# Kernel optimization log

Hardware: AMD Instinct MI355X
Metric: run time of the kernel (lower is better)

Reference implementation:

```python
import jax, jax.numpy as jnp
import numpy as np

B, N, L, M, F = 32, 32, 512, 64, 64
EPS = 1e-8

def setup_inputs() -> dict:
    key = jax.random.key(0)
    k1, k2, k3, k4, k5 = jax.random.split(key, 5)
    x_aug = jax.random.normal(k1, (B, N, L, F), dtype=jnp.float32)
    # monotone time grid in [0,1], shape (L,1) so it broadcasts against (1,N,1,M)
    t = jnp.linspace(0.0, 1.0, L, dtype=jnp.float32)[:, None]
    t_left = jax.random.uniform(k2, (N, M), dtype=jnp.float32) * 0.8
    t_right = t_left + 0.05 + 0.15 * jax.random.uniform(k3, (N, M), dtype=jnp.float32)
    kappa = jax.random.normal(k4, (N, 1), dtype=jnp.float32)
    return {"x_aug": x_aug, "t": t, "t_left": t_left, "t_right": t_right, "kappa": kappa}

def reference(x_aug, t, t_left, t_right, kappa):
    # kappa: (N,1) -> softplus -> (1,N,1,1)
    k = jax.nn.softplus(kappa)[None, :, None]          # (1,N,1,1)
    tl = t_left[None, :, None, :]                       # (1,N,1,M)
    tr = t_right[None, :, None, :]                      # (1,N,1,M)
    # soft box kernel over time: alpha (1,N,L,M)
    alpha = jax.nn.sigmoid((tr - t) / k) * jax.nn.sigmoid((t - tl) / k)
    # weighted pool over L without materializing (B,N,L,M,F)
    numerator = jnp.einsum('bnlf,nlm->bnmf', x_aug, alpha[0])  # (B,N,M,F)
    denominator = alpha.sum(axis=2)[..., None]                 # (1,N,M,1)
    return numerator / (denominator + EPS)
```

## Files before the change

### kernel.cpp

```cpp
#include <hip/hip_runtime.h>
#include <math.h>

typedef unsigned short u16;
typedef unsigned int   u32;
typedef __attribute__((ext_vector_type(8))) short short8;
typedef __attribute__((ext_vector_type(4))) float f32x4;

namespace {
constexpr int Bb = 32, Nn = 32, Ll = 512, Mm = 64, Ff = 64;
constexpr int TL  = 32;
constexpr int NT  = Ll / TL;
constexpr int TLP = 40;
constexpr float EPSV = 1e-8f;
}

__device__ __forceinline__ u16 bf16rne(float x) {
    u32 u = __float_as_uint(x);
    return (u16)((u + 0x7fffu + ((u >> 16) & 1u)) >> 16);
}
__device__ __forceinline__ float bf16tof(u16 h) {
    return __uint_as_float(((u32)h) << 16);
}

__global__ __launch_bounds__(256, 4)
void wagg_fused(const float* __restrict__ x_aug,
                const float* __restrict__ t_in,
                const float* __restrict__ t_left,
                const float* __restrict__ t_right,
                const float* __restrict__ kappa,
                float* __restrict__ out)
{
    const int n   = blockIdx.x & 31;
    const int b   = blockIdx.x >> 5;
    const int tid = threadIdx.x;

    __shared__ u16 ah_s[2][Mm * TLP];
    __shared__ u16 al_s[2][Mm * TLP];
    __shared__ u16 xh_s[2][Ff * TLP];
    __shared__ u16 xl_s[2][Ff * TLP];

    const int fq  = tid & 15;
    const int lp2 = tid >> 4;

    const int wv   = tid >> 6;
    const int lane = tid & 63;
    const int ma   = wv * 16 + (lane >> 2);
    const int lqa  = lane & 3;

    const int mh = wv & 1;
    const int fh = wv >> 1;
    const int q  = lane >> 4;
    const int c  = lane & 15;

    const float* xb = x_aug + (size_t)(b * Nn + n) * (Ll * Ff);

    const float kap = kappa[n];
    const float kk  = fmaxf(kap, 0.0f) + log1pf(expf(-fabsf(kap)));
    const float ik  = 1.0f / kk;
    const float tlv = t_left [n * Mm + ma];
    const float trv = t_right[n * Mm + ma];
    const float Ac  = __expf(-trv * ik);
    const float Bc  = __expf( tlv * ik);

    f32x4 acc[2][2];
    #pragma unroll
    for (int mi = 0; mi < 2; ++mi)
        #pragma unroll
        for (int fi = 0; fi < 2; ++fi)
            acc[mi][fi] = (f32x4){0.f, 0.f, 0.f, 0.f};

    float X0[4], X1[4];
    float T[8];
    float dsum = 0.0f;

    auto stage = [&](int buf) {
        #pragma unroll
        for (int j = 0; j < 4; ++j) {
            const float v0 = X0[j], v1 = X1[j];
            const u16 h0 = bf16rne(v0), h1 = bf16rne(v1);
            const u16 s0 = bf16rne(v0 - bf16tof(h0)), s1 = bf16rne(v1 - bf16tof(h1));
            const u32 off = (u32)(fq * 4 + j) * TLP + 2 * lp2;
            *(u32*)&xh_s[buf][off] = (u32)h0 | ((u32)h1 << 16);
            *(u32*)&xl_s[buf][off] = (u32)s0 | ((u32)s1 << 16);
        }
        u32 hi[4], lo[4];
        #pragma unroll
        for (int jj = 0; jj < 8; jj += 2) {
            const float u0 = __expf(T[jj]     * ik);
            const float u1 = __expf(T[jj + 1] * ik);
            const float d0 = fmaf(Ac, u0, 1.0f) * (u0 + Bc);
            const float d1 = fmaf(Ac, u1, 1.0f) * (u1 + Bc);
            const float a0 = u0 * __builtin_amdgcn_rcpf(d0);
            const float a1 = u1 * __builtin_amdgcn_rcpf(d1);
            dsum += a0 + a1;
            const u16 h0 = bf16rne(a0), h1 = bf16rne(a1);
            const u16 s0 = bf16rne(a0 - bf16tof(h0)), s1 = bf16rne(a1 - bf16tof(h1));
            hi[jj >> 1] = (u32)h0 | ((u32)h1 << 16);
            lo[jj >> 1] = (u32)s0 | ((u32)s1 << 16);
        }
        const u32 aoff = (u32)ma * TLP + lqa * 8;
        *(uint4*)&ah_s[buf][aoff] = make_uint4(hi[0], hi[1], hi[2], hi[3]);
        *(uint4*)&al_s[buf][aoff] = make_uint4(lo[0], lo[1], lo[2], lo[3]);
    };

    {
        const float* p = xb + (size_t)(2 * lp2) * Ff + fq * 4;
        *(float4*)X0 = *(const float4*)p;
        *(float4*)X1 = *(const float4*)(p + Ff);
        *(float4*)&T[0] = *(const float4*)&t_in[lqa * 8];
        *(float4*)&T[4] = *(const float4*)&t_in[lqa * 8 + 4];
        stage(0);
    }
    __syncthreads();

    for (int tile = 0; tile < NT; ++tile) {
        const int cur = tile & 1, nxt = cur ^ 1;

        if (tile + 1 < NT) {
            const int l0 = (tile + 1) * TL;
            const float* p = xb + (size_t)(l0 + 2 * lp2) * Ff + fq * 4;
            *(float4*)X0 = *(const float4*)p;
            *(float4*)X1 = *(const float4*)(p + Ff);
            *(float4*)&T[0] = *(const float4*)&t_in[l0 + lqa * 8];
            *(float4*)&T[4] = *(const float4*)&t_in[l0 + lqa * 8 + 4];
        }

        short8 ahf[2], alf[2], xhf[2], xlf[2];
        #pragma unroll
        for (int mi = 0; mi < 2; ++mi) {
            const u32 off = (u32)(mh * 32 + mi * 16 + c) * TLP + q * 8;
            ahf[mi] = *(const short8*)&ah_s[cur][off];
            alf[mi] = *(const short8*)&al_s[cur][off];
        }
        #pragma unroll
        for (int fi = 0; fi < 2; ++fi) {
            const u32 off = (u32)(fh * 32 + fi * 16 + c) * TLP + q * 8;
            xhf[fi] = *(const short8*)&xh_s[cur][off];
            xlf[fi] = *(const short8*)&xl_s[cur][off];
        }
        #pragma unroll
        for (int mi = 0; mi < 2; ++mi)
            #pragma unroll
            for (int fi = 0; fi < 2; ++fi) {
                acc[mi][fi] = __builtin_amdgcn_mfma_f32_16x16x32_bf16(
                    ahf[mi], xhf[fi], acc[mi][fi], 0, 0, 0);
                acc[mi][fi] = __builtin_amdgcn_mfma_f32_16x16x32_bf16(
                    ahf[mi], xlf[fi], acc[mi][fi], 0, 0, 0);
                acc[mi][fi] = __builtin_amdgcn_mfma_f32_16x16x32_bf16(
                    alf[mi], xhf[fi], acc[mi][fi], 0, 0, 0);
            }

        if (tile + 1 < NT) stage(nxt);
        __syncthreads();
    }

    float* dred = (float*)&xh_s[0][0];
    float* invp = dred + 256;
    dred[lqa * 64 + ma] = dsum;
    __syncthreads();
    if (tid < Mm) {
        const float d = dred[tid] + dred[64 + tid] + dred[128 + tid] + dred[192 + tid];
        invp[tid] = __builtin_amdgcn_rcpf(d + EPSV);
    }
    __syncthreads();

    float* ob = out + (size_t)(b * Nn + n) * (Mm * Ff);
    #pragma unroll
    for (int mi = 0; mi < 2; ++mi) {
        const int mbase = mh * 32 + mi * 16 + q * 4;
        float iv[4];
        #pragma unroll
        for (int r = 0; r < 4; ++r) iv[r] = invp[mbase + r];
        #pragma unroll
        for (int fi = 0; fi < 2; ++fi) {
            const int f = fh * 32 + fi * 16 + c;
            #pragma unroll
            for (int r = 0; r < 4; ++r)
                ob[(size_t)(mbase + r) * Ff + f] = acc[mi][fi][r] * iv[r];
        }
    }
}

extern "C" void kernel_launch(void* const* d_in, const int* in_sizes, int n_in,
                              void* d_out, int out_size, void* d_ws, size_t ws_size,
                              hipStream_t stream)
{
    const float* x_aug   = (const float*)d_in[0];
    const float* t_in    = (const float*)d_in[1];
    const float* t_left  = (const float*)d_in[2];
    const float* t_right = (const float*)d_in[3];
    const float* kappa   = (const float*)d_in[4];
    float* out = (float*)d_out;

    hipLaunchKernelGGL(wagg_fused, dim3(Bb * Nn), dim3(256), 0, stream,
                       x_aug, t_in, t_left, t_right, kappa, out);
}
```

Measured before the change: 205.9 us.

## Precompute alpha split-bf16 tiles in separate kernel and stream them from global memory

Splits the fused kernel in two. A small per-n kernel computes the sigmoid-product weights once, stores them as hi/lo bf16 in an MFMA-fragment-friendly global layout, and stores the reciprocal denominators. The main kernel then loads those fragments directly from global (L2-resident) instead of recomputing alpha in every batch block. It also adds an XOR swizzle on the x LDS tiles, a two-deep register prefetch of x, and a lighter lgkm-only barrier. The cost is an extra launch and a small global workspace round trip, with the fused kernel kept as a fallback when no workspace is provided.

```diff
diff --git a/kernel.cpp b/kernel.cpp
--- a/kernel.cpp
+++ b/kernel.cpp
@@ -12,6 +12,7 @@
 constexpr int NT  = Ll / TL;
 constexpr int TLP = 40;
 constexpr float EPSV = 1e-8f;
+constexpr size_t A_ELEMS = (size_t)Nn * Ll * Mm;
 }
 
 __device__ __forceinline__ u16 bf16rne(float x) {
@@ -22,37 +23,26 @@
     return __uint_as_float(((u32)h) << 16);
 }
 
+__device__ __forceinline__ void lgkm_barrier() {
+    asm volatile("s_waitcnt lgkmcnt(0)" ::: "memory");
+    __builtin_amdgcn_s_barrier();
+    asm volatile("" ::: "memory");
+}
+
 __global__ __launch_bounds__(256, 4)
-void wagg_fused(const float* __restrict__ x_aug,
-                const float* __restrict__ t_in,
+void wagg_alpha(const float* __restrict__ t_in,
                 const float* __restrict__ t_left,
                 const float* __restrict__ t_right,
                 const float* __restrict__ kappa,
-                float* __restrict__ out)
+                u16* __restrict__ Ahi, u16* __restrict__ Alo,
+                float* __restrict__ inv_g)
 {
-    const int n   = blockIdx.x & 31;
-    const int b   = blockIdx.x >> 5;
+    const int n   = blockIdx.x;
     const int tid = threadIdx.x;
-
-    __shared__ u16 ah_s[2][Mm * TLP];
-    __shared__ u16 al_s[2][Mm * TLP];
-    __shared__ u16 xh_s[2][Ff * TLP];
-    __shared__ u16 xl_s[2][Ff * TLP];
-
-    const int fq  = tid & 15;
-    const int lp2 = tid >> 4;
-
-    const int wv   = tid >> 6;
-    const int lane = tid & 63;
-    const int ma   = wv * 16 + (lane >> 2);
-    const int lqa  = lane & 3;
-
-    const int mh = wv & 1;
-    const int fh = wv >> 1;
-    const int q  = lane >> 4;
-    const int c  = lane & 15;
-
-    const float* xb = x_aug + (size_t)(b * Nn + n) * (Ll * Ff);
+    const int ma  = tid >> 2;
+    const int lqa = tid & 3;
+
+    __shared__ float dred[256];
 
     const float kap = kappa[n];
     const float kk  = fmaxf(kap, 0.0f) + log1pf(expf(-fabsf(kap)));
@@ -62,27 +52,11 @@
     const float Ac  = __expf(-trv * ik);
     const float Bc  = __expf( tlv * ik);
 
-    f32x4 acc[2][2];
-    #pragma unroll
-    for (int mi = 0; mi < 2; ++mi)
-        #pragma unroll
-        for (int fi = 0; fi < 2; ++fi)
-            acc[mi][fi] = (f32x4){0.f, 0.f, 0.f, 0.f};
-
-    float X0[4], X1[4];
-    float T[8];
     float dsum = 0.0f;
-
-    auto stage = [&](int buf) {
-        #pragma unroll
-        for (int j = 0; j < 4; ++j) {
-            const float v0 = X0[j], v1 = X1[j];
-            const u16 h0 = bf16rne(v0), h1 = bf16rne(v1);
-            const u16 s0 = bf16rne(v0 - bf16tof(h0)), s1 = bf16rne(v1 - bf16tof(h1));
-            const u32 off = (u32)(fq * 4 + j) * TLP + 2 * lp2;
-            *(u32*)&xh_s[buf][off] = (u32)h0 | ((u32)h1 << 16);
-            *(u32*)&xl_s[buf][off] = (u32)s0 | ((u32)s1 << 16);
-        }
+    for (int t = 0; t < NT; ++t) {
+        float T[8];
+        *(float4*)&T[0] = *(const float4*)&t_in[t * TL + lqa * 8];
+        *(float4*)&T[4] = *(const float4*)&t_in[t * TL + lqa * 8 + 4];
         u32 hi[4], lo[4];
         #pragma unroll
         for (int jj = 0; jj < 8; jj += 2) {
@@ -98,6 +72,201 @@
             hi[jj >> 1] = (u32)h0 | ((u32)h1 << 16);
             lo[jj >> 1] = (u32)s0 | ((u32)s1 << 16);
         }
+        const size_t off = ((((size_t)n * NT + t) * 4 + lqa) * Mm + ma) * 8;
+        *(uint4*)&Ahi[off] = make_uint4(hi[0], hi[1], hi[2], hi[3]);
+        *(uint4*)&Alo[off] = make_uint4(lo[0], lo[1], lo[2], lo[3]);
+    }
+
+    dred[lqa * 64 + ma] = dsum;
+    __syncthreads();
+    if (tid < Mm) {
+        const float d = dred[tid] + dred[64 + tid] + dred[128 + tid] + dred[192 + tid];
+        inv_g[n * Mm + tid] = __builtin_amdgcn_rcpf(d + EPSV);
+    }
+}
+
+__global__ __launch_bounds__(256, 4)
+void wagg_main(const float* __restrict__ x_aug,
+               const u16* __restrict__ Ahi, const u16* __restrict__ Alo,
+               const float* __restrict__ inv_g,
+               float* __restrict__ out)
+{
+    const int n   = blockIdx.x & 31;
+    const int b   = blockIdx.x >> 5;
+    const int tid = threadIdx.x;
+
+    __shared__ u16 xh_s[2][Ff * TLP];
+    __shared__ u16 xl_s[2][Ff * TLP];
+
+    const int fq  = tid & 15;
+    const int lp2 = tid >> 4;
+    const int sw   = (fq >> 1) & 3;
+    const u32 wbase = (u32)(((lp2 >> 2) ^ sw) * 8 + (lp2 & 3) * 2);
+
+    const int wv = tid >> 6, lane = tid & 63;
+    const int mh = wv & 1;
+    const int fh = wv >> 1;
+    const int q  = lane >> 4;
+    const int c  = lane & 15;
+
+    const float* xb = x_aug + (size_t)(b * Nn + n) * (Ll * Ff);
+
+    f32x4 acc[2][2];
+    #pragma unroll
+    for (int mi = 0; mi < 2; ++mi)
+        #pragma unroll
+        for (int fi = 0; fi < 2; ++fi)
+            acc[mi][fi] = (f32x4){0.f, 0.f, 0.f, 0.f};
+
+    float XA0[4], XA1[4], XB0[4], XB1[4];
+
+#define LOADX(X0_, X1_, T_) { \
+    const float* p_ = xb + (size_t)((T_) * TL + 2 * lp2) * Ff + fq * 4; \
+    *(float4*)(X0_) = *(const float4*)p_; \
+    *(float4*)(X1_) = *(const float4*)(p_ + Ff); }
+
+#define STAGEX(BUF_, X0_, X1_) { \
+    _Pragma("unroll") \
+    for (int j = 0; j < 4; ++j) { \
+        const float v0 = (X0_)[j], v1 = (X1_)[j]; \
+        const u16 h0 = bf16rne(v0), h1 = bf16rne(v1); \
+        const u16 s0 = bf16rne(v0 - bf16tof(h0)), s1 = bf16rne(v1 - bf16tof(h1)); \
+        const u32 off_ = (u32)(fq * 4 + j) * TLP + wbase; \
+        *(u32*)&xh_s[BUF_][off_] = (u32)h0 | ((u32)h1 << 16); \
+        *(u32*)&xl_s[BUF_][off_] = (u32)s0 | ((u32)s1 << 16); } }
+
+#define TILE(T_, CUR_, XS0_, XS1_, XL0_, XL1_) { \
+    short8 ahf[2], alf[2], xhf[2], xlf[2]; \
+    const u16* ab_ = Ahi + ((((size_t)n * NT + (T_)) * 4 + q) * Mm) * 8; \
+    const u16* lb_ = Alo + ((((size_t)n * NT + (T_)) * 4 + q) * Mm) * 8; \
+    _Pragma("unroll") \
+    for (int mi = 0; mi < 2; ++mi) { \
+        const int row_ = mh * 32 + mi * 16 + c; \
+        ahf[mi] = *(const short8*)(ab_ + row_ * 8); \
+        alf[mi] = *(const short8*)(lb_ + row_ * 8); } \
+    if ((T_) + 2 < NT) LOADX(XL0_, XL1_, (T_) + 2); \
+    _Pragma("unroll") \
+    for (int fi = 0; fi < 2; ++fi) { \
+        const int row_ = fh * 32 + fi * 16 + c; \
+        const u32 off_ = (u32)row_ * TLP + (u32)((q ^ ((row_ >> 3) & 3)) * 8); \
+        xhf[fi] = *(const short8*)&xh_s[CUR_][off_]; \
+        xlf[fi] = *(const short8*)&xl_s[CUR_][off_]; } \
+    _Pragma("unroll") \
+    for (int mi = 0; mi < 2; ++mi) \
+        _Pragma("unroll") \
+        for (int fi = 0; fi < 2; ++fi) { \
+            acc[mi][fi] = __builtin_amdgcn_mfma_f32_16x16x32_bf16(ahf[mi], xhf[fi], acc[mi][fi], 0, 0, 0); \
+            acc[mi][fi] = __builtin_amdgcn_mfma_f32_16x16x32_bf16(ahf[mi], xlf[fi], acc[mi][fi], 0, 0, 0); \
+            acc[mi][fi] = __builtin_amdgcn_mfma_f32_16x16x32_bf16(alf[mi], xhf[fi], acc[mi][fi], 0, 0, 0); } \
+    if ((T_) + 1 < NT) STAGEX((CUR_) ^ 1, XS0_, XS1_); \
+    lgkm_barrier(); }
+
+    LOADX(XA0, XA1, 0);
+    STAGEX(0, XA0, XA1);
+    LOADX(XB0, XB1, 1);
+    lgkm_barrier();
+
+    for (int tt = 0; tt < NT / 2; ++tt) {
+        const int t0 = 2 * tt;
+        TILE(t0,     0, XB0, XB1, XA0, XA1);
+        TILE(t0 + 1, 1, XA0, XA1, XB0, XB1);
+    }
+
+#undef TILE
+#undef STAGEX
+#undef LOADX
+
+    const float* ivp = inv_g + n * Mm;
+    float* ob = out + (size_t)(b * Nn + n) * (Mm * Ff);
+    #pragma unroll
+    for (int mi = 0; mi < 2; ++mi) {
+        const int mbase = mh * 32 + mi * 16 + q * 4;
+        float iv[4];
+        *(float4*)iv = *(const float4*)&ivp[mbase];
+        #pragma unroll
+        for (int fi = 0; fi < 2; ++fi) {
+            const int f = fh * 32 + fi * 16 + c;
+            #pragma unroll
+            for (int r = 0; r < 4; ++r)
+                ob[(size_t)(mbase + r) * Ff + f] = acc[mi][fi][r] * iv[r];
+        }
+    }
+}
+
+__global__ __launch_bounds__(256, 4)
+void wagg_fused(const float* __restrict__ x_aug,
+                const float* __restrict__ t_in,
+                const float* __restrict__ t_left,
+                const float* __restrict__ t_right,
+                const float* __restrict__ kappa,
+                float* __restrict__ out)
+{
+    const int n   = blockIdx.x & 31;
+    const int b   = blockIdx.x >> 5;
+    const int tid = threadIdx.x;
+
+    __shared__ u16 ah_s[2][Mm * TLP];
+    __shared__ u16 al_s[2][Mm * TLP];
+    __shared__ u16 xh_s[2][Ff * TLP];
+    __shared__ u16 xl_s[2][Ff * TLP];
+
+    const int fq  = tid & 15;
+    const int lp2 = tid >> 4;
+    const int wv   = tid >> 6;
+    const int lane = tid & 63;
+    const int ma   = wv * 16 + (lane >> 2);
+    const int lqa  = lane & 3;
+    const int mh = wv & 1;
+    const int fh = wv >> 1;
+    const int q  = lane >> 4;
+    const int c  = lane & 15;
+
+    const float* xb = x_aug + (size_t)(b * Nn + n) * (Ll * Ff);
+
+    const float kap = kappa[n];
+    const float kk  = fmaxf(kap, 0.0f) + log1pf(expf(-fabsf(kap)));
+    const float ik  = 1.0f / kk;
+    const float tlv = t_left [n * Mm + ma];
+    const float trv = t_right[n * Mm + ma];
+    const float Ac  = __expf(-trv * ik);
+    const float Bc  = __expf( tlv * ik);
+
+    f32x4 acc[2][2];
+    #pragma unroll
+    for (int mi = 0; mi < 2; ++mi)
+        #pragma unroll
+        for (int fi = 0; fi < 2; ++fi)
+            acc[mi][fi] = (f32x4){0.f, 0.f, 0.f, 0.f};
+
+    float X0[4], X1[4];
+    float T[8];
+    float dsum = 0.0f;
+
+    auto stage = [&](int buf) {
+        #pragma unroll
+        for (int j = 0; j < 4; ++j) {
+            const float v0 = X0[j], v1 = X1[j];
+            const u16 h0 = bf16rne(v0), h1 = bf16rne(v1);
+            const u16 s0 = bf16rne(v0 - bf16tof(h0)), s1 = bf16rne(v1 - bf16tof(h1));
+            const u32 off = (u32)(fq * 4 + j) * TLP + 2 * lp2;
+            *(u32*)&xh_s[buf][off] = (u32)h0 | ((u32)h1 << 16);
+            *(u32*)&xl_s[buf][off] = (u32)s0 | ((u32)s1 << 16);
+        }
+        u32 hi[4], lo[4];
+        #pragma unroll
+        for (int jj = 0; jj < 8; jj += 2) {
+            const float u0 = __expf(T[jj]     * ik);
+            const float u1 = __expf(T[jj + 1] * ik);
+            const float d0 = fmaf(Ac, u0, 1.0f) * (u0 + Bc);
+            const float d1 = fmaf(Ac, u1, 1.0f) * (u1 + Bc);
+            const float a0 = u0 * __builtin_amdgcn_rcpf(d0);
+            const float a1 = u1 * __builtin_amdgcn_rcpf(d1);
+            dsum += a0 + a1;
+            const u16 h0 = bf16rne(a0), h1 = bf16rne(a1);
+            const u16 s0 = bf16rne(a0 - bf16tof(h0)), s1 = bf16rne(a1 - bf16tof(h1));
+            hi[jj >> 1] = (u32)h0 | ((u32)h1 << 16);
+            lo[jj >> 1] = (u32)s0 | ((u32)s1 << 16);
+        }
         const u32 aoff = (u32)ma * TLP + lqa * 8;
         *(uint4*)&ah_s[buf][aoff] = make_uint4(hi[0], hi[1], hi[2], hi[3]);
         *(uint4*)&al_s[buf][aoff] = make_uint4(lo[0], lo[1], lo[2], lo[3]);
@@ -192,6 +361,17 @@
     const float* kappa   = (const float*)d_in[4];
     float* out = (float*)d_out;
 
-    hipLaunchKernelGGL(wagg_fused, dim3(Bb * Nn), dim3(256), 0, stream,
-                       x_aug, t_in, t_left, t_right, kappa, out);
-}
+    const size_t need = 2 * A_ELEMS * sizeof(u16) + (size_t)Nn * Mm * sizeof(float);
+    if (d_ws != nullptr && ws_size >= need) {
+        u16*   Ahi   = (u16*)d_ws;
+        u16*   Alo   = Ahi + A_ELEMS;
+        float* inv_g = (float*)(Alo + A_ELEMS);
+        hipLaunchKernelGGL(wagg_alpha, dim3(Nn), dim3(256), 0, stream,
+                           t_in, t_left, t_right, kappa, Ahi, Alo, inv_g);
+        hipLaunchKernelGGL(wagg_main, dim3(Bb * Nn), dim3(256), 0, stream,
+                           x_aug, Ahi, Alo, inv_g, out);
+    } else {
+        hipLaunchKernelGGL(wagg_fused, dim3(Bb * Nn), dim3(256), 0, stream,
+                           x_aug, t_in, t_left, t_right, kappa, out);
+    }
+}
```

Result: slower. 216.7 us (+5.3%).

## Prefetch x two tiles ahead, swizzle x LDS layout, use lighter LDS-only barriers

Applied to the files above, without the earlier changes.

The kernel now issues global loads of x two tiles ahead using two alternating register sets, with the tile loop manually unrolled by two. This gives memory latency more time to hide behind the MFMA work. The LDS layout for the x hi/lo split gets an XOR swizzle on the column chunk to reduce bank conflicts on the transposed writes and fragment reads. __syncthreads is replaced with an lgkmcnt-only wait plus s_barrier, so outstanding global loads no longer drain at every barrier. The cost is higher register pressure from the extra prefetch buffers.

```diff
diff --git a/kernel.cpp b/kernel.cpp
--- a/kernel.cpp
+++ b/kernel.cpp
@@ -22,13 +22,19 @@
     return __uint_as_float(((u32)h) << 16);
 }
 
+__device__ __forceinline__ void lgkm_barrier() {
+    asm volatile("s_waitcnt lgkmcnt(0)" ::: "memory");
+    __builtin_amdgcn_s_barrier();
+    asm volatile("" ::: "memory");
+}
+
 __global__ __launch_bounds__(256, 4)
-void wagg_fused(const float* __restrict__ x_aug,
-                const float* __restrict__ t_in,
-                const float* __restrict__ t_left,
-                const float* __restrict__ t_right,
-                const float* __restrict__ kappa,
-                float* __restrict__ out)
+void wagg_fused2(const float* __restrict__ x_aug,
+                 const float* __restrict__ t_in,
+                 const float* __restrict__ t_left,
+                 const float* __restrict__ t_right,
+                 const float* __restrict__ kappa,
+                 float* __restrict__ out)
 {
     const int n   = blockIdx.x & 31;
     const int b   = blockIdx.x >> 5;
@@ -41,6 +47,8 @@
 
     const int fq  = tid & 15;
     const int lp2 = tid >> 4;
+    const int sw    = (fq >> 1) & 3;
+    const u32 wbase = (u32)(((lp2 >> 2) ^ sw) * 8 + (lp2 & 3) * 2);
 
     const int wv   = tid >> 6;
     const int lane = tid & 63;
@@ -69,100 +77,97 @@
         for (int fi = 0; fi < 2; ++fi)
             acc[mi][fi] = (f32x4){0.f, 0.f, 0.f, 0.f};
 
-    float X0[4], X1[4];
+    float XA0[4], XA1[4], XB0[4], XB1[4];
     float T[8];
     float dsum = 0.0f;
 
-    auto stage = [&](int buf) {
-        #pragma unroll
-        for (int j = 0; j < 4; ++j) {
-            const float v0 = X0[j], v1 = X1[j];
-            const u16 h0 = bf16rne(v0), h1 = bf16rne(v1);
-            const u16 s0 = bf16rne(v0 - bf16tof(h0)), s1 = bf16rne(v1 - bf16tof(h1));
-            const u32 off = (u32)(fq * 4 + j) * TLP + 2 * lp2;
-            *(u32*)&xh_s[buf][off] = (u32)h0 | ((u32)h1 << 16);
-            *(u32*)&xl_s[buf][off] = (u32)s0 | ((u32)s1 << 16);
-        }
-        u32 hi[4], lo[4];
-        #pragma unroll
-        for (int jj = 0; jj < 8; jj += 2) {
-            const float u0 = __expf(T[jj]     * ik);
-            const float u1 = __expf(T[jj + 1] * ik);
-            const float d0 = fmaf(Ac, u0, 1.0f) * (u0 + Bc);
-            const float d1 = fmaf(Ac, u1, 1.0f) * (u1 + Bc);
-            const float a0 = u0 * __builtin_amdgcn_rcpf(d0);
-            const float a1 = u1 * __builtin_amdgcn_rcpf(d1);
-            dsum += a0 + a1;
-            const u16 h0 = bf16rne(a0), h1 = bf16rne(a1);
-            const u16 s0 = bf16rne(a0 - bf16tof(h0)), s1 = bf16rne(a1 - bf16tof(h1));
-            hi[jj >> 1] = (u32)h0 | ((u32)h1 << 16);
-            lo[jj >> 1] = (u32)s0 | ((u32)s1 << 16);
-        }
-        const u32 aoff = (u32)ma * TLP + lqa * 8;
-        *(uint4*)&ah_s[buf][aoff] = make_uint4(hi[0], hi[1], hi[2], hi[3]);
-        *(uint4*)&al_s[buf][aoff] = make_uint4(lo[0], lo[1], lo[2], lo[3]);
-    };
-
-    {
-        const float* p = xb + (size_t)(2 * lp2) * Ff + fq * 4;
-        *(float4*)X0 = *(const float4*)p;
-        *(float4*)X1 = *(const float4*)(p + Ff);
-        *(float4*)&T[0] = *(const float4*)&t_in[lqa * 8];
-        *(float4*)&T[4] = *(const float4*)&t_in[lqa * 8 + 4];
-        stage(0);
+#define LOADX(X0_, X1_, T_) { \
+    const float* p_ = xb + (size_t)((T_) * TL + 2 * lp2) * Ff + fq * 4; \
+    *(float4*)(X0_) = *(const float4*)p_; \
+    *(float4*)(X1_) = *(const float4*)(p_ + Ff); }
+
+#define LOADT(T_) { \
+    *(float4*)&T[0] = *(const float4*)&t_in[(T_) * TL + lqa * 8]; \
+    *(float4*)&T[4] = *(const float4*)&t_in[(T_) * TL + lqa * 8 + 4]; }
+
+#define STAGEX(BUF_, X0_, X1_) { \
+    _Pragma("unroll") \
+    for (int j = 0; j < 4; ++j) { \
+        const float v0 = (X0_)[j], v1 = (X1_)[j]; \
+        const u16 h0 = bf16rne(v0), h1 = bf16rne(v1); \
+        const u16 s0 = bf16rne(v0 - bf16tof(h0)), s1 = bf16rne(v1 - bf16tof(h1)); \
+        const u32 off_ = (u32)(fq * 4 + j) * TLP + wbase; \
+        *(u32*)&xh_s[BUF_][off_] = (u32)h0 | ((u32)h1 << 16); \
+        *(u32*)&xl_s[BUF_][off_] = (u32)s0 | ((u32)s1 << 16); } \
+    u32 hi_[4], lo_[4]; \
+    _Pragma("unroll") \
+    for (int jj = 0; jj < 8; jj += 2) { \
+        const float u0 = __expf(T[jj]     * ik); \
+        const float u1 = __expf(T[jj + 1] * ik); \
+        const float d0 = fmaf(Ac, u0, 1.0f) * (u0 + Bc); \
+        const float d1 = fmaf(Ac, u1, 1.0f) * (u1 + Bc); \
+        const float a0 = u0 * __builtin_amdgcn_rcpf(d0); \
+        const float a1 = u1 * __builtin_amdgcn_rcpf(d1); \
+        dsum += a0 + a1; \
+        const u16 h0 = bf16rne(a0), h1 = bf16rne(a1); \
+        const u16 s0 = bf16rne(a0 - bf16tof(h0)), s1 = bf16rne(a1 - bf16tof(h1)); \
+        hi_[jj >> 1] = (u32)h0 | ((u32)h1 << 16); \
+        lo_[jj >> 1] = (u32)s0 | ((u32)s1 << 16); } \
+    const u32 aoff_ = (u32)ma * TLP + lqa * 8; \
+    *(uint4*)&ah_s[BUF_][aoff_] = make_uint4(hi_[0], hi_[1], hi_[2], hi_[3]); \
+    *(uint4*)&al_s[BUF_][aoff_] = make_uint4(lo_[0], lo_[1], lo_[2], lo_[3]); }
+
+#define TILE(T_, CUR_, XS0_, XS1_, XL0_, XL1_) { \
+    if ((T_) + 1 < NT) LOADT((T_) + 1); \
+    if ((T_) + 2 < NT) LOADX(XL0_, XL1_, (T_) + 2); \
+    short8 ahf[2], alf[2], xhf[2], xlf[2]; \
+    _Pragma("unroll") \
+    for (int mi = 0; mi < 2; ++mi) { \
+        const u32 off_ = (u32)(mh * 32 + mi * 16 + c) * TLP + q * 8; \
+        ahf[mi] = *(const short8*)&ah_s[CUR_][off_]; \
+        alf[mi] = *(const short8*)&al_s[CUR_][off_]; } \
+    _Pragma("unroll") \
+    for (int fi = 0; fi < 2; ++fi) { \
+        const int row_ = fh * 32 + fi * 16 + c; \
+        const u32 off_ = (u32)row_ * TLP + (u32)((q ^ ((row_ >> 3) & 3)) * 8); \
+        xhf[fi] = *(const short8*)&xh_s[CUR_][off_]; \
+        xlf[fi] = *(const short8*)&xl_s[CUR_][off_]; } \
+    _Pragma("unroll") \
+    for (int mi = 0; mi < 2; ++mi) \
+        _Pragma("unroll") \
+        for (int fi = 0; fi < 2; ++fi) { \
+            acc[mi][fi] = __builtin_amdgcn_mfma_f32_16x16x32_bf16(ahf[mi], xhf[fi], acc[mi][fi], 0, 0, 0); \
+            acc[mi][fi] = __builtin_amdgcn_mfma_f32_16x16x32_bf16(ahf[mi], xlf[fi], acc[mi][fi], 0, 0, 0); \
+            acc[mi][fi] = __builtin_amdgcn_mfma_f32_16x16x32_bf16(alf[mi], xhf[fi], acc[mi][fi], 0, 0, 0); } \
+    if ((T_) + 1 < NT) STAGEX((CUR_) ^ 1, XS0_, XS1_); \
+    lgkm_barrier(); }
+
+    LOADX(XA0, XA1, 0);
+    LOADT(0);
+    STAGEX(0, XA0, XA1);
+    LOADX(XB0, XB1, 1);
+    lgkm_barrier();
+
+    for (int tt = 0; tt < NT / 2; ++tt) {
+        const int t0 = 2 * tt;
+        TILE(t0,     0, XB0, XB1, XA0, XA1);
+        TILE(t0 + 1, 1, XA0, XA1, XB0, XB1);
     }
-    __syncthreads();
-
-    for (int tile = 0; tile < NT; ++tile) {
-        const int cur = tile & 1, nxt = cur ^ 1;
-
-        if (tile + 1 < NT) {
-            const int l0 = (tile + 1) * TL;
-            const float* p = xb + (size_t)(l0 + 2 * lp2) * Ff + fq * 4;
-            *(float4*)X0 = *(const float4*)p;
-            *(float4*)X1 = *(const float4*)(p + Ff);
-            *(float4*)&T[0] = *(const float4*)&t_in[l0 + lqa * 8];
-            *(float4*)&T[4] = *(const float4*)&t_in[l0 + lqa * 8 + 4];
-        }
-
-        short8 ahf[2], alf[2], xhf[2], xlf[2];
-        #pragma unroll
-        for (int mi = 0; mi < 2; ++mi) {
-            const u32 off = (u32)(mh * 32 + mi * 16 + c) * TLP + q * 8;
-            ahf[mi] = *(const short8*)&ah_s[cur][off];
-            alf[mi] = *(const short8*)&al_s[cur][off];
-        }
-        #pragma unroll
-        for (int fi = 0; fi < 2; ++fi) {
-            const u32 off = (u32)(fh * 32 + fi * 16 + c) * TLP + q * 8;
-            xhf[fi] = *(const short8*)&xh_s[cur][off];
-            xlf[fi] = *(const short8*)&xl_s[cur][off];
-        }
-        #pragma unroll
-        for (int mi = 0; mi < 2; ++mi)
-            #pragma unroll
-            for (int fi = 0; fi < 2; ++fi) {
-                acc[mi][fi] = __builtin_amdgcn_mfma_f32_16x16x32_bf16(
-                    ahf[mi], xhf[fi], acc[mi][fi], 0, 0, 0);
-                acc[mi][fi] = __builtin_amdgcn_mfma_f32_16x16x32_bf16(
-                    ahf[mi], xlf[fi], acc[mi][fi], 0, 0, 0);
-                acc[mi][fi] = __builtin_amdgcn_mfma_f32_16x16x32_bf16(
-                    alf[mi], xhf[fi], acc[mi][fi], 0, 0, 0);
-            }
-
-        if (tile + 1 < NT) stage(nxt);
-        __syncthreads();
-    }
+
+#undef TILE
+#undef STAGEX
+#undef LOADT
+#undef LOADX
 
     float* dred = (float*)&xh_s[0][0];
     float* invp = dred + 256;
     dred[lqa * 64 + ma] = dsum;
-    __syncthreads();
+    lgkm_barrier();
     if (tid < Mm) {
         const float d = dred[tid] + dred[64 + tid] + dred[128 + tid] + dred[192 + tid];
         invp[tid] = __builtin_amdgcn_rcpf(d + EPSV);
     }
-    __syncthreads();
+    lgkm_barrier();
 
     float* ob = out + (size_t)(b * Nn + n) * (Mm * Ff);
     #pragma unroll
@@ -192,6 +197,6 @@
     const float* kappa   = (const float*)d_in[4];
     float* out = (float*)d_out;
 
-    hipLaunchKernelGGL(wagg_fused, dim3(Bb * Nn), dim3(256), 0, stream,
+    hipLaunchKernelGGL(wagg_fused2, dim3(Bb * Nn), dim3(256), 0, stream,
                        x_aug, t_in, t_left, t_right, kappa, out);
 }
```

Result: no change. 207.2 us (+0.7%).
